# Kernel optimization log

Hardware: AMD Instinct MI355X
Metric: run time of the kernel (lower is better)

## Reference

```python
import jax, jax.numpy as jnp
import numpy as np

P = 8  # patch size
EPS = 1e-5

def ln_ch(x, w, b):
    # WithBias LayerNorm over channel dim of (B,C,H,W): torch code flattens to (B,HW,C) and norms last dim
    mu = x.mean(axis=1, keepdims=True)
    var = ((x - mu) ** 2).mean(axis=1, keepdims=True)
    return (x - mu) / jnp.sqrt(var + EPS) * w[None, :, None, None] + b[None, :, None, None]

def conv1x1(x, w):
    # w: [C_out, C_in]
    return jnp.einsum('bchw,oc->bohw', x, w)

def dwconv3x3(x, w):
    # depthwise 3x3, w: [C,1,3,3]
    return jax.lax.conv_general_dilated(x, w, (1, 1), 'SAME', dimension_numbers=('NCHW', 'OIHW', 'NCHW'), feature_group_count=x.shape[1])

def patchify(x):
    b, c, H, W = x.shape
    return x.reshape(b, c, H // P, P, W // P, P).transpose(0, 1, 2, 4, 3, 5)  # b c h w p1 p2

def unpatchify(x):
    b, c, h, w, p1, p2 = x.shape
    return x.transpose(0, 1, 2, 4, 3, 5).reshape(b, c, h * p1, w * p2)

def setup_inputs() -> dict:
    key = jax.random.key(0)
    ks = jax.random.split(key, 16)
    B, C, H, W = 4, 64, 256, 256
    hid = 2 * C  # ffn_expansion_factor=2
    s = 0.02
    return {
        'x': jax.random.normal(ks[0], (B, C, H, W), jnp.float32),
        'evt': jax.random.normal(ks[1], (B, C, H, W), jnp.float32),
        'ln1i_w': jnp.ones((C,), jnp.float32), 'ln1i_b': jnp.zeros((C,), jnp.float32),
        'ln1e_w': jnp.ones((C,), jnp.float32), 'ln1e_b': jnp.zeros((C,), jnp.float32),
        'w_q': jax.random.normal(ks[2], (2 * C, C), jnp.float32) * s,
        'dw_q': jax.random.normal(ks[3], (2 * C, 1, 3, 3), jnp.float32) * s,
        'w_kv': jax.random.normal(ks[4], (4 * C, C), jnp.float32) * s,
        'dw_kv': jax.random.normal(ks[5], (4 * C, 1, 3, 3), jnp.float32) * s,
        'lnA_w': jnp.ones((2 * C,), jnp.float32), 'lnA_b': jnp.zeros((2 * C,), jnp.float32),
        'w_po_attn': jax.random.normal(ks[6], (C, 2 * C), jnp.float32) * s,
        'ln2_w': jnp.ones((C,), jnp.float32), 'ln2_b': jnp.zeros((C,), jnp.float32),
        'w_pi': jax.random.normal(ks[7], (2 * hid, C), jnp.float32) * s,
        'fft_param': jnp.ones((2 * hid, 1, 1, P, P // 2 + 1), jnp.float32),
        'dw_ffn': jax.random.normal(ks[8], (2 * hid, 1, 3, 3), jnp.float32) * s,
        'w_po_ffn': jax.random.normal(ks[9], (C, hid), jnp.float32) * s,
    }

def reference(x, evt, ln1i_w, ln1i_b, ln1e_w, ln1e_b, w_q, dw_q, w_kv, dw_kv, lnA_w, lnA_b, w_po_attn, ln2_w, ln2_b, w_pi, fft_param, dw_ffn, w_po_ffn):
    # ---- EventFSAS cross attention ----
    xn = ln_ch(x, ln1i_w, ln1i_b)
    en = ln_ch(evt, ln1e_w, ln1e_b)
    q = dwconv3x3(conv1x1(xn, w_q), dw_q)               # (B,2C,H,W)
    kv = dwconv3x3(conv1x1(en, w_kv), dw_kv)            # (B,4C,H,W)
    k, v = jnp.split(kv, 2, axis=1)
    qf = jnp.fft.rfft2(patchify(q))                      # (B,2C,h,w,8,5) complex
    kf = jnp.fft.rfft2(patchify(k))
    out = jnp.fft.irfft2(qf * kf, s=(P, P))
    out = ln_ch(unpatchify(out), lnA_w, lnA_b)
    x = x + conv1x1(v * out, w_po_attn)
    # ---- DFFN ----
    y = conv1x1(ln_ch(x, ln2_w, ln2_b), w_pi)            # (B,4C,H,W)
    yf = jnp.fft.rfft2(patchify(y)) * fft_param
    y = unpatchify(jnp.fft.irfft2(yf, s=(P, P)))
    y = dwconv3x3(y, dw_ffn)
    y1, y2 = jnp.split(y, 2, axis=1)
    y = jax.nn.gelu(y1, approximate=False) * y2          # torch nn.GELU is exact erf form
    return x + conv1x1(y, w_po_ffn)
```

## Files before the change

kernel.cpp:

```cpp
#include <hip/hip_runtime.h>

#define HW 65536
#define NPOS 262144

typedef unsigned int   u32;
typedef unsigned short u16;
typedef __attribute__((ext_vector_type(8))) short v8s;
typedef __attribute__((ext_vector_type(4))) float f32x4;
typedef __attribute__((ext_vector_type(2))) float f32x2;

__device__ __forceinline__ float bf2f(u16 h){
  union { u32 u; float f; } c; c.u = ((u32)h) << 16; return c.f;
}
__device__ __forceinline__ u16 f2bf(float f){
  union { u32 u; float f; } c; c.f = f;
  u32 r = c.u + 0x7fffu + ((c.u >> 16) & 1u);
  return (u16)(r >> 16);
}
__device__ __forceinline__ u32 pk2(float a, float b){
  return (u32)f2bf(a) | ((u32)f2bf(b) << 16);
}
__device__ __forceinline__ v8s as8(uint4 u){
  union { uint4 a; v8s b; } c; c.a = u; return c.b;
}
__device__ __forceinline__ f32x2 up2(u32 u){
  union { u32 u; float f; } lo, hi;
  lo.u = u << 16; hi.u = u & 0xffff0000u;
  f32x2 r; r.x = lo.f; r.y = hi.f; return r;
}
__device__ __forceinline__ float gelu_exact(float x){
  return 0.5f*x*(1.0f+erff(x*0.70710678118654752f));
}

__device__ void fold_w(const float* __restrict__ W, int rows,
                       const float* __restrict__ lw, const float* __restrict__ lb,
                       u16* __restrict__ Wf, float* __restrict__ A, float* __restrict__ B){
  int tid = threadIdx.x;
  for (int e = tid; e < rows*64; e += 256) Wf[e] = f2bf(lw[e & 63] * W[e]);
  for (int r = tid; r < rows; r += 256){
    float a = 0.f, b2 = 0.f;
    for (int c = 0; c < 64; c++){ float w = W[r*64+c]; a += lw[c]*w; b2 += lb[c]*w; }
    A[r] = a; B[r] = b2;
  }
}

__global__ void k_prep(const float* __restrict__ M, float* __restrict__ g,
    const float* wq,  const float* l1iw, const float* l1ib, u16* wqf,  float* aq,  float* bq,
    const float* wkv, const float* l1ew, const float* l1eb, u16* wkvf, float* akv, float* bkv,
    const float* wpi, const float* l2w,  const float* l2b,  u16* wpif, float* api, float* bpi,
    const float* wpa, u16* wpaf, const float* wpf, u16* wpff)
{
  int blk = blockIdx.x, tid = threadIdx.x;
  if (blk < 64){
    int t = blk*256 + tid;
    int c = t >> 6, uv = t & 63, u = uv >> 3, v = uv & 7;
    const float* mc = M + c*40;
    const float ctab[8] = {1.f, 0.70710678118654752f, 0.f, -0.70710678118654752f,
                           -1.f, -0.70710678118654752f, 0.f, 0.70710678118654752f};
    float acc = 0.f;
    for (int k1=0;k1<8;k1++)
      for (int k2=0;k2<8;k2++){
        float s = (k2<=4) ? mc[k1*5+k2] : mc[(((8-k1)&7)*5) + (8-k2)];
        acc += s * ctab[(k1*u + k2*v)&7];
      }
    g[t] = acc * (1.f/64.f);
  } else if (blk == 64){ fold_w(wq, 128, l1iw, l1ib, wqf, aq, bq); }
  else if (blk == 65){ fold_w(wkv, 256, l1ew, l1eb, wkvf, akv, bkv); }
  else if (blk == 66){ fold_w(wpi, 256, l2w, l2b, wpif, api, bpi); }
  else if (blk == 67){ for (int e=tid; e<64*128; e+=256) wpaf[e] = f2bf(wpa[e]); }
  else               { for (int e=tid; e<64*128; e+=256) wpff[e] = f2bf(wpf[e]); }
}

__global__ void k_prep2(const float* __restrict__ g, u16* __restrict__ CM){
  int c = blockIdx.x;
  const float* gc = g + (size_t)c*64;
  u16* cm = CM + (size_t)c*4096;
  for (int e = threadIdx.x; e < 4096; e += 256){
    int o = e >> 6, i = e & 63;
    int du = ((o>>3) - (i>>3)) & 7, dv = ((o&7) - (i&7)) & 7;
    cm[e] = f2bf(gc[du*8 + dv]);
  }
}

struct GA {
  const float* src; const u16* Wf; const float* Af; const float* Bf;
  u32* dst; int o0; int dstOffP; int Cdp; int b0; int pxbase;
};

template<int NZ>
__global__ __launch_bounds__(256) void k_gemm64(GA a0, GA a1){
  GA a = (blockIdx.y == 0) ? a0 : a1;
  __shared__ uint4 lsX[128*8];
  __shared__ uint4 lsW[64*NZ*8];
  __shared__ float2 sPart[256];
  __shared__ float2 sStat[128];
  int tid = threadIdx.x;
  int px = tid & 127, hf = tid >> 7;
  int p0 = a.pxbase + blockIdx.x*128;
  int b = p0 >> 16, hwb = p0 & 65535;
  {
    const uint4* wsrc = (const uint4*)(a.Wf + (size_t)a.o0*64);
    #pragma unroll
    for (int i=0; i<NZ*2; i++){
      int idx = i*256 + tid, row = idx>>3, s = idx&7;
      lsW[row*8 + (s ^ (row&7))] = wsrc[idx];
    }
  }
  {
    const float* sp = a.src + (size_t)b*64*HW + hwb + px + (size_t)(hf*32)*HW;
    float e[32];
    #pragma unroll
    for (int c=0;c<32;c++) e[c] = sp[(size_t)c*HW];
    float sm = 0.f, sq = 0.f;
    #pragma unroll
    for (int c=0;c<32;c++){ sm += e[c]; sq += e[c]*e[c]; }
    uint4* xrow = lsX + px*8;
    #pragma unroll
    for (int sl=0; sl<4; sl++){
      uint4 pkv;
      pkv.x = pk2(e[sl*8+0], e[sl*8+1]); pkv.y = pk2(e[sl*8+2], e[sl*8+3]);
      pkv.z = pk2(e[sl*8+4], e[sl*8+5]); pkv.w = pk2(e[sl*8+6], e[sl*8+7]);
      xrow[(hf*4+sl) ^ (px&7)] = pkv;
    }
    sPart[tid] = make_float2(sm, sq);
  }
  __syncthreads();
  if (tid < 128){
    float2 A = sPart[tid], B = sPart[tid+128];
    float s = A.x + B.x, q = A.y + B.y;
    float mu = s*(1.f/64.f);
    float var = q*(1.f/64.f) - mu*mu;
    sStat[tid] = make_float2(mu, rsqrtf(fmaxf(var,0.f)+1e-5f));
  }
  __syncthreads();
  int w = tid>>6, l = tid&63, g = l>>4, c15 = l&15;
  float2 stv[2];
  #pragma unroll
  for (int pp=0;pp<2;pp++) stv[pp] = sStat[w*32 + pp*16 + c15];

  #pragma unroll
  for (int z=0; z<NZ; z++){
    f32x4 acc[2][4];
    #pragma unroll
    for (int pp=0;pp<2;pp++)
      #pragma unroll
      for (int po=0;po<4;po++) acc[pp][po] = (f32x4){0.f,0.f,0.f,0.f};
    #pragma unroll
    for (int kk=0; kk<2; kk++){
      v8s wf[4], xf[2];
      #pragma unroll
      for (int po=0;po<4;po++){ int row = z*64 + po*16 + c15; wf[po] = as8(lsW[row*8 + ((kk*4+g) ^ (row&7))]); }
      #pragma unroll
      for (int pp=0;pp<2;pp++){ int row = w*32 + pp*16 + c15; xf[pp] = as8(lsX[row*8 + ((kk*4+g) ^ (row&7))]); }
      #pragma unroll
      for (int pp=0;pp<2;pp++)
        #pragma unroll
        for (int po=0;po<4;po++)
          acc[pp][po] = __builtin_amdgcn_mfma_f32_16x16x32_bf16(wf[po], xf[pp], acc[pp][po], 0,0,0);
    }
    size_t obaseP = ((size_t)(b - a.b0)*a.Cdp + a.dstOffP + z*32)*HW + hwb + w*32;
    #pragma unroll
    for (int po=0;po<4;po++)
      #pragma unroll
      for (int j2=0;j2<2;j2++){
        int oc = po*16 + g*4 + j2*2;
        float A0 = a.Af[a.o0 + z*64 + oc],   B0 = a.Bf[a.o0 + z*64 + oc];
        float A1 = a.Af[a.o0 + z*64 + oc+1], B1 = a.Bf[a.o0 + z*64 + oc+1];
        int ocp = po*8 + g*2 + j2;
        u32* dp = a.dst + obaseP + (size_t)ocp*HW + c15;
        #pragma unroll
        for (int pp=0;pp<2;pp++){
          float lo = stv[pp].y*(acc[pp][po][j2*2  ] - stv[pp].x*A0) + B0;
          float hi = stv[pp].y*(acc[pp][po][j2*2+1] - stv[pp].x*A1) + B1;
          dp[pp*16] = pk2(lo, hi);
        }
      }
  }
}

__global__ __launch_bounds__(256) void k_gemm_attn(
    const float* __restrict__ x, const u32* __restrict__ orawp, const u32* __restrict__ vbp,
    const float* __restrict__ lnw, const float* __restrict__ lnb,
    const u16* __restrict__ Wf, float* __restrict__ out)
{
  __shared__ uint4 lsX[128*16];
  __shared__ uint4 lsW[64*16];
  __shared__ float2 sPart[256];
  __shared__ float2 sStat[128];
  int tid = threadIdx.x;
  int p0 = blockIdx.x*128;
  int b = p0 >> 16, hwb = p0 & 65535;
  int px = tid & 127, hf = tid >> 7;
  {
    const uint4* wsrc = (const uint4*)Wf;
    #pragma unroll
    for (int i=0;i<4;i++){
      int idx = i*256 + tid, row = idx>>4, s = idx&15;
      lsW[row*16 + (s ^ (row&15))] = wsrc[idx];
    }
  }
  const u32* orp = orawp + ((size_t)b*64 + hf*32)*HW + hwb + px;
  {
    u32 r32[32];
    #pragma unroll
    for (int i=0;i<32;i++) r32[i] = orp[(size_t)i*HW];
    float sum = 0.f, ssq = 0.f;
    #pragma unroll
    for (int sl=0; sl<8; sl++){
      u32 wds[4];
      #pragma unroll
      for (int q2=0;q2<4;q2++){
        u32 wv = r32[sl*4+q2];
        float fl = bf2f((u16)(wv&0xffff)), fh = bf2f((u16)(wv>>16));
        sum += fl + fh; ssq += fl*fl + fh*fh;
        wds[q2] = wv;
      }
      int s = hf*8 + sl;
      lsX[px*16 + (s ^ (px&15))] = make_uint4(wds[0],wds[1],wds[2],wds[3]);
    }
    sPart[tid] = make_float2(sum, ssq);
  }
  __syncthreads();
  if (tid < 128){
    float2 A = sPart[tid], B = sPart[tid+128];
    float s = A.x + B.x, q = A.y + B.y;
    float mu = s*(1.f/128.f);
    float var = q*(1.f/128.f) - mu*mu;
    sStat[tid] = make_float2(mu, rsqrtf(fmaxf(var,0.f)+1e-5f));
  }
  __syncthreads();
  {
    float2 st = sStat[px];
    const u32* vp = vbp + ((size_t)b*64 + hf*32)*HW + hwb + px;
    u32 v32[32];
    #pragma unroll
    for (int i=0;i<32;i++) v32[i] = vp[(size_t)i*HW];
    #pragma unroll
    for (int sl=0; sl<8; sl++){
      int s = hf*8 + sl;
      int li = px*16 + (s ^ (px&15));
      uint4 raw = lsX[li];
      u32 wds[4] = {raw.x, raw.y, raw.z, raw.w};
      u32 ow[4];
      #pragma unroll
      for (int q2=0;q2<4;q2++){
        int ch = hf*64 + sl*8 + q2*2;
        float e0 = bf2f((u16)(wds[q2]&0xffff)), e1 = bf2f((u16)(wds[q2]>>16));
        u32 vv = v32[sl*4+q2];
        float v0 = bf2f((u16)(vv&0xffff)), v1 = bf2f((u16)(vv>>16));
        float r0 = ((e0-st.x)*st.y*lnw[ch  ] + lnb[ch  ])*v0;
        float r1 = ((e1-st.x)*st.y*lnw[ch+1] + lnb[ch+1])*v1;
        ow[q2] = pk2(r0, r1);
      }
      lsX[li] = make_uint4(ow[0],ow[1],ow[2],ow[3]);
    }
  }
  __syncthreads();
  int w4 = tid>>6, l = tid&63, g = l>>4, c15 = l&15;
  f32x4 acc[2][4];
  #pragma unroll
  for (int pp=0;pp<2;pp++)
    #pragma unroll
    for (int po=0;po<4;po++) acc[pp][po] = (f32x4){0.f,0.f,0.f,0.f};
  #pragma unroll
  for (int kk=0; kk<4; kk++){
    v8s wf[4], xf[2];
    #pragma unroll
    for (int po=0;po<4;po++){ int row = po*16 + c15; wf[po] = as8(lsW[row*16 + ((kk*4+g) ^ (row&15))]); }
    #pragma unroll
    for (int pp=0;pp<2;pp++){ int row = w4*32 + pp*16 + c15; xf[pp] = as8(lsX[row*16 + ((kk*4+g) ^ (row&15))]); }
    #pragma unroll
    for (int pp=0;pp<2;pp++)
      #pragma unroll
      for (int po=0;po<4;po++)
        acc[pp][po] = __builtin_amdgcn_mfma_f32_16x16x32_bf16(wf[po], xf[pp], acc[pp][po], 0,0,0);
  }
  size_t obase = (size_t)b*64*HW + hwb + w4*32;
  #pragma unroll
  for (int po=0;po<4;po++)
    #pragma unroll
    for (int j=0;j<4;j++){
      int oc = po*16 + g*4 + j;
      const float* xs = x + obase + (size_t)oc*HW + c15;
      float* dp = out + obase + (size_t)oc*HW + c15;
      #pragma unroll
      for (int pp=0;pp<2;pp++) dp[pp*16] = xs[pp*16] + acc[pp][po][j];
    }
}

__global__ __launch_bounds__(256) void k_gemm_ffn(
    const u32* __restrict__ y3gp, const u16* __restrict__ Wf, float* __restrict__ out,
    int pxbase, int b0)
{
  __shared__ uint4 lsX[128*16];
  __shared__ uint4 lsW[64*16];
  int tid = threadIdx.x;
  int p0 = pxbase + blockIdx.x*128;
  int b = p0 >> 16, hwb = p0 & 65535;
  int px = tid & 127, hf = tid >> 7;
  {
    const uint4* wsrc = (const uint4*)Wf;
    #pragma unroll
    for (int i=0;i<4;i++){
      int idx = i*256 + tid, row = idx>>4, s = idx&15;
      lsW[row*16 + (s ^ (row&15))] = wsrc[idx];
    }
  }
  const u32* yp = y3gp + ((size_t)(b-b0)*64 + hf*32)*HW + hwb + px;
  {
    u32 r32[32];
    #pragma unroll
    for (int i=0;i<32;i++) r32[i] = yp[(size_t)i*HW];
    #pragma unroll
    for (int sl=0; sl<8; sl++){
      int s = hf*8 + sl;
      lsX[px*16 + (s ^ (px&15))] = make_uint4(r32[sl*4+0],r32[sl*4+1],r32[sl*4+2],r32[sl*4+3]);
    }
  }
  __syncthreads();
  int w4 = tid>>6, l = tid&63, g = l>>4, c15 = l&15;
  f32x4 acc[2][4];
  #pragma unroll
  for (int pp=0;pp<2;pp++)
    #pragma unroll
    for (int po=0;po<4;po++) acc[pp][po] = (f32x4){0.f,0.f,0.f,0.f};
  #pragma unroll
  for (int kk=0; kk<4; kk++){
    v8s wf[4], xf[2];
    #pragma unroll
    for (int po=0;po<4;po++){ int row = po*16 + c15; wf[po] = as8(lsW[row*16 + ((kk*4+g) ^ (row&15))]); }
    #pragma unroll
    for (int pp=0;pp<2;pp++){ int row = w4*32 + pp*16 + c15; xf[pp] = as8(lsX[row*16 + ((kk*4+g) ^ (row&15))]); }
    #pragma unroll
    for (int pp=0;pp<2;pp++)
      #pragma unroll
      for (int po=0;po<4;po++)
        acc[pp][po] = __builtin_amdgcn_mfma_f32_16x16x32_bf16(wf[po], xf[pp], acc[pp][po], 0,0,0);
  }
  size_t obase = (size_t)b*64*HW + hwb + w4*32;
  #pragma unroll
  for (int po=0;po<4;po++)
    #pragma unroll
    for (int j=0;j<4;j++){
      int oc = po*16 + g*4 + j;
      float* dp = out + obase + (size_t)oc*HW + c15;
      #pragma unroll
      for (int pp=0;pp<2;pp++) dp[pp*16] = dp[pp*16] + acc[pp][po][j];
    }
}

__device__ __forceinline__ void dw8p_acc2(const u32* __restrict__ sp,
    const float* __restrict__ w9lo, const float* __restrict__ w9hi,
    int h, int w8, f32x2 a2[8])
{
  #pragma unroll
  for (int r=0;r<3;r++){
    int hh = h + r - 1;
    if (hh < 0 || hh > 255) continue;
    const u32* rp = sp + hh*256 + w8;
    uint4 ua = *(const uint4*)rp;
    uint4 ub = *(const uint4*)(rp+4);
    u32 e[8] = {ua.x,ua.y,ua.z,ua.w,ub.x,ub.y,ub.z,ub.w};
    u32 lef = (w8 > 0)   ? rp[-1] : 0u;
    u32 rig = (w8 < 248) ? rp[8]  : 0u;
    f32x2 vm[10];
    vm[0] = up2(lef);
    #pragma unroll
    for (int j=0;j<8;j++) vm[j+1] = up2(e[j]);
    vm[9] = up2(rig);
    f32x2 wa = {w9lo[r*3  ], w9hi[r*3  ]};
    f32x2 wb = {w9lo[r*3+1], w9hi[r*3+1]};
    f32x2 wc = {w9lo[r*3+2], w9hi[r*3+2]};
    #pragma unroll
    for (int j=0;j<8;j++)
      a2[j] += vm[j]*wa + vm[j+1]*wb + vm[j+2]*wc;
  }
}

__device__ __forceinline__ void rfft8(const f32x2 x[8], f32x2 F[8]){
  f32x2 E0 = x[0]+x[2]+x[4]+x[6];
  f32x2 E2 = x[0]-x[2]+x[4]-x[6];
  f32x2 E1r = x[0]-x[4], E1i = x[6]-x[2];
  f32x2 O0 = x[1]+x[3]+x[5]+x[7];
  f32x2 O2 = x[1]-x[3]+x[5]-x[7];
  f32x2 O1r = x[1]-x[5], O1i = x[7]-x[3];
  const float C = 0.70710678118654752f;
  f32x2 s = (O1r+O1i)*C, d = (O1i-O1r)*C;
  F[0] = E0+O0;
  F[1] = E1r+s;  F[2] = E1i+d;
  F[3] = E2;     F[4] = -O2;
  F[5] = E1r-s;  F[6] = d-E1i;
  F[7] = E0-O0;
}

__global__ __launch_bounds__(256) void k_dw8p(
    const u32* __restrict__ src, const float* __restrict__ wgt, int c0,
    u32* __restrict__ dstp, int dstOffP, int prMask, int prShift, int srcStride, int srcBase)
{
  int t = blockIdx.x*256 + threadIdx.x;
  int w8 = (t & 31)*8, h = (t>>5) & 255;
  int plane = t >> 13;
  int pr = plane & prMask, b = plane >> prShift;
  const u32* sp = src + ((size_t)(b*srcStride + srcBase + pr))*HW;
  const float* w9 = wgt + (size_t)(c0 + 2*pr)*9;
  f32x2 a2[8];
  #pragma unroll
  for (int j=0;j<8;j++) a2[j] = (f32x2){0.f,0.f};
  dw8p_acc2(sp, w9, w9+9, h, w8, a2);
  u32* dp = dstp + ((size_t)(b*64 + dstOffP + pr))*HW + h*256 + w8;
  uint4 s0, s1;
  s0.x=pk2(a2[0].x,a2[0].y); s0.y=pk2(a2[1].x,a2[1].y); s0.z=pk2(a2[2].x,a2[2].y); s0.w=pk2(a2[3].x,a2[3].y);
  s1.x=pk2(a2[4].x,a2[4].y); s1.y=pk2(a2[5].x,a2[5].y); s1.z=pk2(a2[6].x,a2[6].y); s1.w=pk2(a2[7].x,a2[7].y);
  *(uint4*)dp = s0; *(uint4*)(dp+4) = s1;
}

__global__ __launch_bounds__(256) void k_dw8gp(
    const u32* __restrict__ Y0p, const float* __restrict__ wgt, u32* __restrict__ Y3gp)
{
  int t = blockIdx.x*256 + threadIdx.x;
  int w8 = (t & 31)*8, h = (t>>5) & 255;
  int pc = t >> 13;
  int pr = pc & 63, bl = pc >> 6;
  const u32* spA = Y0p + ((size_t)(bl*128 + pr))*HW;
  const u32* spG = Y0p + ((size_t)(bl*128 + 64 + pr))*HW;
  const float* w9a = wgt + (size_t)(2*pr)*9;
  const float* w9g = wgt + (size_t)(128 + 2*pr)*9;
  f32x2 aA[8], aG[8];
  #pragma unroll
  for (int j=0;j<8;j++){ aA[j] = (f32x2){0.f,0.f}; aG[j] = (f32x2){0.f,0.f}; }
  dw8p_acc2(spA, w9a, w9a+9, h, w8, aA);
  dw8p_acc2(spG, w9g, w9g+9, h, w8, aG);
  u32* dp = Y3gp + ((size_t)(bl*64 + pr))*HW + h*256 + w8;
  uint4 s0, s1;
  s0.x=pk2(gelu_exact(aA[0].x)*aG[0].x, gelu_exact(aA[0].y)*aG[0].y);
  s0.y=pk2(gelu_exact(aA[1].x)*aG[1].x, gelu_exact(aA[1].y)*aG[1].y);
  s0.z=pk2(gelu_exact(aA[2].x)*aG[2].x, gelu_exact(aA[2].y)*aG[2].y);
  s0.w=pk2(gelu_exact(aA[3].x)*aG[3].x, gelu_exact(aA[3].y)*aG[3].y);
  s1.x=pk2(gelu_exact(aA[4].x)*aG[4].x, gelu_exact(aA[4].y)*aG[4].y);
  s1.y=pk2(gelu_exact(aA[5].x)*aG[5].x, gelu_exact(aA[5].y)*aG[5].y);
  s1.z=pk2(gelu_exact(aA[6].x)*aG[6].x, gelu_exact(aA[6].y)*aG[6].y);
  s1.w=pk2(gelu_exact(aA[7].x)*aG[7].x, gelu_exact(aA[7].y)*aG[7].y);
  *(uint4*)dp = s0; *(uint4*)(dp+4) = s1;
}

__global__ __launch_bounds__(256) void k_circqk4(
    const u32* __restrict__ bq, const u32* __restrict__ bk,
    const float* __restrict__ dwq, const float* __restrict__ dwk, int c0,
    u32* __restrict__ orawp, int oprBase, int cpb)
{
  __shared__ f32x2 qd[8][288];
  __shared__ f32x2 kd[8][288];
  int tid = threadIdx.x;
  int p = tid & 31, i = tid >> 5;
  int pr = blockIdx.y, b = blockIdx.z;
  int h0 = blockIdx.x*8;
  const u32* qp = bq + ((size_t)(b*cpb+pr))*HW;
  const u32* kp = bk + ((size_t)(b*cpb+pr))*HW;
  const float* wq9 = dwq + (size_t)(c0 + 2*pr)*9;
  const float* wk9 = dwk + (size_t)(c0 + 2*pr)*9;
  {
    f32x2 a2[8], F[8];
    #pragma unroll
    for (int j=0;j<8;j++) a2[j] = (f32x2){0.f,0.f};
    dw8p_acc2(qp, wq9, wq9+9, h0+i, p*8, a2);
    rfft8(a2, F);
    #pragma unroll
    for (int j=0;j<8;j++) qd[i][p*9+j] = F[j];
  }
  {
    f32x2 a2[8], F[8];
    #pragma unroll
    for (int j=0;j<8;j++) a2[j] = (f32x2){0.f,0.f};
    dw8p_acc2(kp, wk9, wk9+9, h0+i, p*8, a2);
    rfft8(a2, F);
    #pragma unroll
    for (int j=0;j<8;j++) kd[i][p*9+j] = F[j];
  }
  __syncthreads();
  f32x2 A[8];
  #pragma unroll
  for (int j=0;j<8;j++) A[j] = (f32x2){0.f,0.f};
  #pragma unroll
  for (int u=0;u<8;u++){
    int ku = (i-u)&7;
    const f32x2* Q = &qd[u][p*9];
    const f32x2* K = &kd[ku][p*9];
    f32x2 q0=Q[0],q1=Q[1],q2=Q[2],q3=Q[3],q4=Q[4],q5=Q[5],q6=Q[6],q7=Q[7];
    f32x2 k0=K[0],k1=K[1],k2=K[2],k3=K[3],k4=K[4],k5=K[5],k6=K[6],k7=K[7];
    A[0] += q0*k0;
    A[1] += q1*k1 - q2*k2;  A[2] += q1*k2 + q2*k1;
    A[3] += q3*k3 - q4*k4;  A[4] += q3*k4 + q4*k3;
    A[5] += q5*k5 - q6*k6;  A[6] += q5*k6 + q6*k5;
    A[7] += q7*k7;
  }
  const float C = 0.70710678118654752f;
  const float IV = 0.125f;
  f32x2 a0=A[0], b4=A[7], r1=A[1], i1=A[2], r2=A[3], i2=A[4], r3=A[5], i3=A[6];
  f32x2 t0 = a0+b4, t1 = a0-b4;
  f32x2 o[8];
  o[0] = (t0 + (r1+r2+r3)*2.f)*IV;
  o[1] = (t1 + ((r1-i1)*C - i2 - (r3+i3)*C)*2.f)*IV;
  o[2] = (t0 + (i3-i1-r2)*2.f)*IV;
  o[3] = (t1 + (i2 - (r1+i1)*C + (r3-i3)*C)*2.f)*IV;
  o[4] = (t0 + (r2-r1-r3)*2.f)*IV;
  o[5] = (t1 + ((i1-r1)*C - i2 + (r3+i3)*C)*2.f)*IV;
  o[6] = (t0 + (i1-r2-i3)*2.f)*IV;
  o[7] = (t1 + ((r1+i1)*C + i2 + (i3-r3)*C)*2.f)*IV;
  u32* op = orawp + ((size_t)(b*64 + oprBase + pr))*HW + (size_t)(h0+i)*256 + p*8;
  uint4 s0, s1;
  s0.x=pk2(o[0].x,o[0].y); s0.y=pk2(o[1].x,o[1].y); s0.z=pk2(o[2].x,o[2].y); s0.w=pk2(o[3].x,o[3].y);
  s1.x=pk2(o[4].x,o[4].y); s1.y=pk2(o[5].x,o[5].y); s1.z=pk2(o[6].x,o[6].y); s1.w=pk2(o[7].x,o[7].y);
  *(uint4*)op = s0; *(uint4*)(op+4) = s1;
}

__global__ __launch_bounds__(256) void k_circg_mfma(
    u32* __restrict__ y, const u16* __restrict__ CM)
{
  __shared__ uint4 lsA[2][64*8];
  __shared__ uint4 lsB[2][64*8];
  int tid = threadIdx.x;
  int pr = blockIdx.y, b = blockIdx.z;
  int h0 = blockIdx.x*16;
  u32* plane = y + ((size_t)(b*128+pr))*HW;
  {
    const uint4* cmsrc = (const uint4*)(CM + (size_t)(2*pr)*4096);
    #pragma unroll
    for (int t=0; t<4; t++){
      int idx = t*256 + tid;
      int ch = idx >> 9, e = idx & 511;
      int row = e >> 3, s = e & 7;
      lsA[ch][row*8 + (s ^ (row&7))] = cmsrc[ch*512 + e];
    }
  }
  {
    #pragma unroll
    for (int t=0; t<2; t++){
      int rr = t*256 + tid;
      int n = rr >> 3, i = rr & 7;
      const u32* rp = plane + (size_t)(h0 + (n>>5)*8 + i)*256 + (n&31)*8;
      uint4 ua = *(const uint4*)rp;
      uint4 ub = *(const uint4*)(rp+4);
      u32 e[8] = {ua.x,ua.y,ua.z,ua.w,ub.x,ub.y,ub.z,ub.w};
      uint4 L, H;
      L.x = (e[0]&0xffffu) | (e[1]<<16);
      L.y = (e[2]&0xffffu) | (e[3]<<16);
      L.z = (e[4]&0xffffu) | (e[5]<<16);
      L.w = (e[6]&0xffffu) | (e[7]<<16);
      H.x = (e[0]>>16) | (e[1]&0xffff0000u);
      H.y = (e[2]>>16) | (e[3]&0xffff0000u);
      H.z = (e[4]>>16) | (e[5]&0xffff0000u);
      H.w = (e[6]>>16) | (e[7]&0xffff0000u);
      lsB[0][n*8 + (i ^ (n&7))] = L;
      lsB[1][n*8 + (i ^ (n&7))] = H;
    }
  }
  __syncthreads();
  int w = tid>>6, l = tid&63, g = l>>4, c15 = l&15;
  f32x4 acc[2][4];
  #pragma unroll
  for (int ch=0;ch<2;ch++)
    #pragma unroll
    for (int po=0;po<4;po++) acc[ch][po] = (f32x4){0.f,0.f,0.f,0.f};
  #pragma unroll
  for (int kk=0; kk<2; kk++){
    v8s bfr[2];
    { int row = w*16 + c15;
      bfr[0] = as8(lsB[0][row*8 + ((kk*4+g) ^ (row&7))]);
      bfr[1] = as8(lsB[1][row*8 + ((kk*4+g) ^ (row&7))]); }
    #pragma unroll
    for (int po=0;po<4;po++){
      int row = po*16 + c15;
      v8s aL = as8(lsA[0][row*8 + ((kk*4+g) ^ (row&7))]);
      v8s aH = as8(lsA[1][row*8 + ((kk*4+g) ^ (row&7))]);
      acc[0][po] = __builtin_amdgcn_mfma_f32_16x16x32_bf16(aL, bfr[0], acc[0][po], 0,0,0);
      acc[1][po] = __builtin_amdgcn_mfma_f32_16x16x32_bf16(aH, bfr[1], acc[1][po], 0,0,0);
    }
  }
  int patch = w*16 + c15;
  u32* pbase = plane + (size_t)(h0 + (patch>>5)*8)*256 + (patch&31)*8;
  #pragma unroll
  for (int po=0;po<4;po++){
    int oh = po*2 + (g>>1), ow4 = 4*(g&1);
    uint4 sv;
    sv.x = pk2(acc[0][po][0], acc[1][po][0]);
    sv.y = pk2(acc[0][po][1], acc[1][po][1]);
    sv.z = pk2(acc[0][po][2], acc[1][po][2]);
    sv.w = pk2(acc[0][po][3], acc[1][po][3]);
    *(uint4*)(pbase + (size_t)oh*256 + ow4) = sv;
  }
}

extern "C" void kernel_launch(void* const* d_in, const int* in_sizes, int n_in,
                              void* d_out, int out_size, void* d_ws, size_t ws_size,
                              hipStream_t stream)
{
  const float* x       = (const float*)d_in[0];
  const float* evt     = (const float*)d_in[1];
  const float* ln1i_w  = (const float*)d_in[2];
  const float* ln1i_b  = (const float*)d_in[3];
  const float* ln1e_w  = (const float*)d_in[4];
  const float* ln1e_b  = (const float*)d_in[5];
  const float* w_q     = (const float*)d_in[6];
  const float* dw_q    = (const float*)d_in[7];
  const float* w_kv    = (const float*)d_in[8];
  const float* dw_kv   = (const float*)d_in[9];
  const float* lnA_w   = (const float*)d_in[10];
  const float* lnA_b   = (const float*)d_in[11];
  const float* w_po_at = (const float*)d_in[12];
  const float* ln2_w   = (const float*)d_in[13];
  const float* ln2_b   = (const float*)d_in[14];
  const float* w_pi    = (const float*)d_in[15];
  const float* fft_par = (const float*)d_in[16];
  const float* dw_ffn  = (const float*)d_in[17];
  const float* w_poffn = (const float*)d_in[18];
  float* out = (float*)d_out;

  char* ws = (char*)d_ws;
  const size_t MiB = 1048576ull;
  bool big = (ws_size >= 200*MiB);
  size_t smOff = big ? 192*MiB : 160*MiB;
  char* sm = ws + smOff;
  float* G    = (float*)(sm);
  u16* WQF    = (u16*)(sm + 65536);
  u16* WKVF   = (u16*)(sm + 81920);
  u16* WPIF   = (u16*)(sm + 114688);
  u16* WPAF   = (u16*)(sm + 147456);
  u16* WPFF   = (u16*)(sm + 163840);
  float* AQ   = (float*)(sm + 180224);
  float* BQ   = (float*)(sm + 180736);
  float* AKV  = (float*)(sm + 181248);
  float* BKV  = (float*)(sm + 182272);
  float* API  = (float*)(sm + 183296);
  float* BPI  = (float*)(sm + 184320);
  u16* CMAT   = (u16*)(sm + 1*MiB);

  dim3 blk256(256);

  k_prep<<<69, blk256, 0, stream>>>(fft_par, G,
      w_q, ln1i_w, ln1i_b, WQF, AQ, BQ,
      w_kv, ln1e_w, ln1e_b, WKVF, AKV, BKV,
      w_pi, ln2_w, ln2_b, WPIF, API, BPI,
      w_po_at, WPAF, w_poffn, WPFF);
  k_prep2<<<256, blk256, 0, stream>>>(G, CMAT);

  if (big){
    u32* QBUF  = (u32*)(ws);
    u32* KBUF  = (u32*)(ws + 64*MiB);
    u32* ORAWp = (u32*)(ws + 128*MiB);
    u32* PV    = (u32*)(ws + 64*MiB);
    u32* VBUFp = (u32*)(ws);
    u32* Y0p   = (u32*)(ws);
    u32* Y3Gp  = (u32*)(ws + 128*MiB);

    GA qa = {x,   WQF,  AQ,  BQ,  QBUF, 0, 0, 64, 0, 0};
    GA ka = {evt, WKVF, AKV, BKV, KBUF, 0, 0, 64, 0, 0};
    k_gemm64<2><<<dim3(2048,2,1), blk256, 0, stream>>>(qa, ka);
    k_circqk4<<<dim3(32,64,4), blk256, 0, stream>>>(QBUF, KBUF, dw_q, dw_kv, 0, ORAWp, 0, 64);
    GA va = {evt, WKVF, AKV, BKV, PV, 128, 0, 64, 0, 0};
    k_gemm64<2><<<dim3(2048,1,1), blk256, 0, stream>>>(va, va);
    k_dw8p<<<8192, blk256, 0, stream>>>(PV, dw_kv, 128, VBUFp, 0, 63, 6, 64, 0);
    k_gemm_attn<<<2048, blk256, 0, stream>>>(x, ORAWp, VBUFp, lnA_w, lnA_b, WPAF, out);
    GA pa = {out, WPIF, API, BPI, Y0p, 0, 0, 128, 0, 0};
    k_gemm64<4><<<dim3(2048,1,1), blk256, 0, stream>>>(pa, pa);
    k_circg_mfma<<<dim3(16,128,4), blk256, 0, stream>>>(Y0p, CMAT);
    k_dw8gp<<<8192, blk256, 0, stream>>>(Y0p, dw_ffn, Y3Gp);
    k_gemm_ffn<<<2048, blk256, 0, stream>>>(Y3Gp, WPFF, out, 0, 0);
  } else {
    u32* P1p   = (u32*)(ws);
    u32* ORAWp = (u32*)(ws + 32*MiB);
    u32* P2p   = (u32*)(ws + 96*MiB);
    u32* VBUFp = (u32*)(ws + 96*MiB);
    u32* Y0p   = (u32*)(ws);
    u32* Y3Gp  = (u32*)(ws + 64*MiB);

    for (int i=0;i<2;i++){
      GA qa = {x,   WQF,  AQ,  BQ,  P1p, 64*i, 0, 32, 0, 0};
      GA ka = {evt, WKVF, AKV, BKV, P2p, 64*i, 0, 32, 0, 0};
      k_gemm64<1><<<dim3(2048,2,1), blk256, 0, stream>>>(qa, ka);
      k_circqk4<<<dim3(32,32,4), blk256, 0, stream>>>(P1p, P2p, dw_q, dw_kv, 64*i, ORAWp, 32*i, 32);
    }
    for (int i=0;i<2;i++){
      GA va = {evt, WKVF, AKV, BKV, P1p, 128+64*i, 0, 32, 0, 0};
      k_gemm64<1><<<dim3(2048,1,1), blk256, 0, stream>>>(va, va);
      k_dw8p<<<4096, blk256, 0, stream>>>(P1p, dw_kv, 128+64*i, VBUFp, 32*i, 31, 5, 32, 0);
    }
    k_gemm_attn<<<2048, blk256, 0, stream>>>(x, ORAWp, VBUFp, lnA_w, lnA_b, WPAF, out);
    for (int h=0;h<2;h++){
      GA pa = {out, WPIF, API, BPI, Y0p, 0, 0, 128, 2*h, h*131072};
      k_gemm64<4><<<dim3(1024,1,1), blk256, 0, stream>>>(pa, pa);
      k_circg_mfma<<<dim3(16,128,2), blk256, 0, stream>>>(Y0p, CMAT);
      k_dw8gp<<<4096, blk256, 0, stream>>>(Y0p, dw_ffn, Y3Gp);
      k_gemm_ffn<<<1024, blk256, 0, stream>>>(Y3Gp, WPFF, out, h*131072, 2*h);
    }
  }
}
```

Measured before the change: 449.8 us.

## Replace direct row circular convolution with FFT along patch-row axis

The per-frequency circular convolution across the 8 patch rows was computed directly, with each thread doing 8 complex multiply-accumulates from shared memory. It now runs a length-8 FFT over the row axis, does a pointwise product and an inverse FFT, with 128 of the 256 threads handling column-frequency components and writing results back to shared memory. After an added barrier, every thread applies the inverse row DFT. This cuts shared-memory reads and arithmetic, but adds a synchronisation and leaves half the threads idle during the FFT stage.

```diff
diff --git a/kernel.cpp b/kernel.cpp
--- a/kernel.cpp
+++ b/kernel.cpp
@@ -393,6 +393,61 @@
   F[7] = E0-O0;
 }
 
+__device__ __forceinline__ void hprod8(const f32x2 a[8], const f32x2 b[8], f32x2 c[8]){
+  c[0] = a[0]*b[0];
+  c[1] = a[1]*b[1] - a[2]*b[2];  c[2] = a[1]*b[2] + a[2]*b[1];
+  c[3] = a[3]*b[3] - a[4]*b[4];  c[4] = a[3]*b[4] + a[4]*b[3];
+  c[5] = a[5]*b[5] - a[6]*b[6];  c[6] = a[5]*b[6] + a[6]*b[5];
+  c[7] = a[7]*b[7];
+}
+
+__device__ __forceinline__ void ridft8(const f32x2 A[8], f32x2 o[8]){
+  const float C = 0.70710678118654752f;
+  const float IV = 0.125f;
+  f32x2 a0=A[0], b4=A[7], r1=A[1], i1=A[2], r2=A[3], i2=A[4], r3=A[5], i3=A[6];
+  f32x2 t0 = a0+b4, t1 = a0-b4;
+  o[0] = (t0 + (r1+r2+r3)*2.f)*IV;
+  o[1] = (t1 + ((r1-i1)*C - i2 - (r3+i3)*C)*2.f)*IV;
+  o[2] = (t0 + (i3-i1-r2)*2.f)*IV;
+  o[3] = (t1 + (i2 - (r1+i1)*C + (r3-i3)*C)*2.f)*IV;
+  o[4] = (t0 + (r2-r1-r3)*2.f)*IV;
+  o[5] = (t1 + ((i1-r1)*C - i2 + (r3+i3)*C)*2.f)*IV;
+  o[6] = (t0 + (i1-r2-i3)*2.f)*IV;
+  o[7] = (t1 + ((r1+i1)*C + i2 + (i3-r3)*C)*2.f)*IV;
+}
+
+__device__ __forceinline__ void cfft8(const f32x2 re[8], const f32x2 im[8],
+                                      f32x2 Rr[8], f32x2 Ri[8]){
+  const float C = 0.70710678118654752f;
+  f32x2 et0r = re[0]+re[4], et0i = im[0]+im[4];
+  f32x2 et1r = re[0]-re[4], et1i = im[0]-im[4];
+  f32x2 et2r = re[2]+re[6], et2i = im[2]+im[6];
+  f32x2 et3r = re[2]-re[6], et3i = im[2]-im[6];
+  f32x2 E0r = et0r+et2r, E0i = et0i+et2i;
+  f32x2 E2r = et0r-et2r, E2i = et0i-et2i;
+  f32x2 E1r = et1r+et3i, E1i = et1i-et3r;
+  f32x2 E3r = et1r-et3i, E3i = et1i+et3r;
+  f32x2 ot0r = re[1]+re[5], ot0i = im[1]+im[5];
+  f32x2 ot1r = re[1]-re[5], ot1i = im[1]-im[5];
+  f32x2 ot2r = re[3]+re[7], ot2i = im[3]+im[7];
+  f32x2 ot3r = re[3]-re[7], ot3i = im[3]-im[7];
+  f32x2 O0r = ot0r+ot2r, O0i = ot0i+ot2i;
+  f32x2 O2r = ot0r-ot2r, O2i = ot0i-ot2i;
+  f32x2 O1r = ot1r+ot3i, O1i = ot1i-ot3r;
+  f32x2 O3r = ot1r-ot3i, O3i = ot1i+ot3r;
+  f32x2 T1r = (O1r+O1i)*C, T1i = (O1i-O1r)*C;
+  f32x2 T2r = O2i,          T2i = -O2r;
+  f32x2 T3r = (O3i-O3r)*C,  T3i = -(O3r+O3i)*C;
+  Rr[0]=E0r+O0r; Ri[0]=E0i+O0i;
+  Rr[4]=E0r-O0r; Ri[4]=E0i-O0i;
+  Rr[1]=E1r+T1r; Ri[1]=E1i+T1i;
+  Rr[5]=E1r-T1r; Ri[5]=E1i-T1i;
+  Rr[2]=E2r+T2r; Ri[2]=E2i+T2i;
+  Rr[6]=E2r-T2r; Ri[6]=E2i-T2i;
+  Rr[3]=E3r+T3r; Ri[3]=E3i+T3i;
+  Rr[7]=E3r-T3r; Ri[7]=E3i-T3i;
+}
+
 __global__ __launch_bounds__(256) void k_dw8p(
     const u32* __restrict__ src, const float* __restrict__ wgt, int c0,
     u32* __restrict__ dstp, int dstOffP, int prMask, int prShift, int srcStride, int srcBase)
@@ -477,35 +532,56 @@
     for (int j=0;j<8;j++) kd[i][p*9+j] = F[j];
   }
   __syncthreads();
-  f32x2 A[8];
-  #pragma unroll
-  for (int j=0;j<8;j++) A[j] = (f32x2){0.f,0.f};
-  #pragma unroll
-  for (int u=0;u<8;u++){
-    int ku = (i-u)&7;
-    const f32x2* Q = &qd[u][p*9];
-    const f32x2* K = &kd[ku][p*9];
-    f32x2 q0=Q[0],q1=Q[1],q2=Q[2],q3=Q[3],q4=Q[4],q5=Q[5],q6=Q[6],q7=Q[7];
-    f32x2 k0=K[0],k1=K[1],k2=K[2],k3=K[3],k4=K[4],k5=K[5],k6=K[6],k7=K[7];
-    A[0] += q0*k0;
-    A[1] += q1*k1 - q2*k2;  A[2] += q1*k2 + q2*k1;
-    A[3] += q3*k3 - q4*k4;  A[4] += q3*k4 + q4*k3;
-    A[5] += q5*k5 - q6*k6;  A[6] += q5*k6 + q6*k5;
-    A[7] += q7*k7;
-  }
-  const float C = 0.70710678118654752f;
-  const float IV = 0.125f;
-  f32x2 a0=A[0], b4=A[7], r1=A[1], i1=A[2], r2=A[3], i2=A[4], r3=A[5], i3=A[6];
-  f32x2 t0 = a0+b4, t1 = a0-b4;
-  f32x2 o[8];
-  o[0] = (t0 + (r1+r2+r3)*2.f)*IV;
-  o[1] = (t1 + ((r1-i1)*C - i2 - (r3+i3)*C)*2.f)*IV;
-  o[2] = (t0 + (i3-i1-r2)*2.f)*IV;
-  o[3] = (t1 + (i2 - (r1+i1)*C + (r3-i3)*C)*2.f)*IV;
-  o[4] = (t0 + (r2-r1-r3)*2.f)*IV;
-  o[5] = (t1 + ((i1-r1)*C - i2 + (r3+i3)*C)*2.f)*IV;
-  o[6] = (t0 + (i1-r2-i3)*2.f)*IV;
-  o[7] = (t1 + ((r1+i1)*C + i2 + (i3-r3)*C)*2.f)*IV;
+  {
+    int c = tid >> 6;
+    int pp = tid & 63;
+    if (pp < 32){
+      if (c == 0){
+        #pragma unroll
+        for (int cc=0; cc<2; cc++){
+          int comp = cc ? 7 : 0;
+          f32x2 cq[8], ck[8], Fq[8], Fk[8], P[8], o[8];
+          #pragma unroll
+          for (int u=0;u<8;u++){ cq[u]=qd[u][pp*9+comp]; ck[u]=kd[u][pp*9+comp]; }
+          rfft8(cq, Fq);
+          rfft8(ck, Fk);
+          hprod8(Fq, Fk, P);
+          ridft8(P, o);
+          #pragma unroll
+          for (int u=0;u<8;u++) qd[u][pp*9+comp] = o[u];
+        }
+      } else {
+        int cr = 2*c-1, cim = 2*c;
+        f32x2 Qr[8],Qi[8],Kr[8],Ki[8];
+        #pragma unroll
+        for (int u=0;u<8;u++){
+          Qr[u]=qd[u][pp*9+cr]; Qi[u]=qd[u][pp*9+cim];
+          Kr[u]=kd[u][pp*9+cr]; Ki[u]=kd[u][pp*9+cim];
+        }
+        f32x2 QR[8],QI[8],KR[8],KI[8];
+        cfft8(Qr,Qi,QR,QI);
+        cfft8(Kr,Ki,KR,KI);
+        f32x2 Wr[8],Wi[8];
+        #pragma unroll
+        for (int v=0;v<8;v++){
+          Wr[v] = QR[v]*KR[v] - QI[v]*KI[v];
+          Wi[v] = QR[v]*KI[v] + QI[v]*KR[v];
+        }
+        f32x2 Dr[8],Di[8];
+        cfft8(Wi,Wr,Dr,Di);
+        #pragma unroll
+        for (int u=0;u<8;u++){
+          qd[u][pp*9+cr]  = Di[u]*0.125f;
+          qd[u][pp*9+cim] = Dr[u]*0.125f;
+        }
+      }
+    }
+  }
+  __syncthreads();
+  f32x2 A[8], o[8];
+  #pragma unroll
+  for (int j=0;j<8;j++) A[j] = qd[i][p*9+j];
+  ridft8(A, o);
   u32* op = orawp + ((size_t)(b*64 + oprBase + pr))*HW + (size_t)(h0+i)*256 + p*8;
   uint4 s0, s1;
   s0.x=pk2(o[0].x,o[0].y); s0.y=pk2(o[1].x,o[1].y); s0.z=pk2(o[2].x,o[2].y); s0.w=pk2(o[3].x,o[3].y);
```

Result: no change. 454.9 us (+1.1%).
